# Kernel tuning notes

Hardware: AMD Instinct MI355X
Metric: run time of the kernel (lower is better)

The kernel has to match this reference:

```python
import jax, jax.numpy as jnp
import numpy as np

N_NODES = 50000
N_EDGES = 1_600_000
IN_DIM = 128
HID = 32
HEADS = 4
NEG_SLOPE = 0.2


def setup_inputs() -> dict:
    key = jax.random.key(0)
    ks = jax.random.split(key, 6)
    h = jax.random.normal(ks[0], (N_NODES, IN_DIM), dtype=jnp.float32)
    src = jax.random.randint(ks[1], (N_EDGES,), 0, N_NODES, dtype=jnp.int32)
    dst = jax.random.randint(ks[2], (N_EDGES,), 0, N_NODES, dtype=jnp.int32)
    s = 1.0 / np.sqrt(IN_DIM)  # ~ Linear default init scale
    Wq = (jax.random.normal(ks[3], (HEADS, IN_DIM, HID), dtype=jnp.float32) * s)
    Wk = (jax.random.normal(ks[4], (HEADS, IN_DIM, HID), dtype=jnp.float32) * s)
    Wv = (jax.random.normal(ks[5], (HEADS, IN_DIM, HID), dtype=jnp.float32) * s)
    return {"h": h, "src": src, "dst": dst, "Wq": Wq, "Wk": Wk, "Wv": Wv}


def _gat_forward(h, src, dst, Wq, Wk, Wv):
    n = h.shape[0]
    # per-head projections: [H, N, D]
    q = jnp.einsum('ni,hio->hno', h, Wq)
    k = jnp.einsum('ni,hio->hno', h, Wk)
    v = jnp.einsum('ni,hio->hno', h, Wv)
    # edge scores: e = leaky_relu(<q_src, k_dst>)  -> [H, E]
    e = jax.nn.leaky_relu(jnp.einsum('hed,hed->he', q[:, src], k[:, dst]),
                          negative_slope=NEG_SLOPE)
    # segment softmax over incoming edges of each dst node
    seg_max = jax.vmap(lambda x: jax.ops.segment_max(x, dst, num_segments=n))(e)
    seg_max = jax.lax.stop_gradient(jnp.where(jnp.isfinite(seg_max), seg_max, 0.0))
    ex = jnp.exp(e - seg_max[:, dst])                       # [H, E]
    denom = jax.vmap(lambda x: jax.ops.segment_sum(x, dst, num_segments=n))(ex)
    alpha = ex / jnp.maximum(denom, 1e-9)[:, dst]           # [H, E]
    # weighted scatter-sum of source values into dst nodes: [H, N, D]
    msg = alpha[..., None] * v[:, src]
    out = jax.vmap(lambda m: jax.ops.segment_sum(m, dst, num_segments=n))(msg)
    # concat heads along feature dim -> [N, H*D]
    return out.transpose(1, 0, 2).reshape(n, HEADS * HID)


def reference(h, src, dst, Wq, Wk, Wv):
    return _gat_forward(h, src, dst, Wq, Wk, Wv)
```

## Files before the change

### kernel.cpp

```cpp
#include <hip/hip_runtime.h>
#include <hip/hip_fp16.h>

#define IN_DIM 128
#define HID 32
#define HEADS 4
#define OUTC (HEADS*HID)
#define NEG_SLOPE 0.2f
#define BSH 4
#define BN 16
#define BCAP 768
#define NBMAX 3200
#define NCOLS 384
#define WPB 192
#define NP 25
#define PSH 11
#define PCAP 72704
#define PBLK 18
#define OSTRIDE 392

typedef _Float16 f16x8 __attribute__((ext_vector_type(8)));
typedef float    f32x4 __attribute__((ext_vector_type(4)));

__device__ __forceinline__ unsigned short f2h(float f) {
    return __half_as_ushort(__float2half_rn(f));
}
__device__ __forceinline__ float2 h2f2(unsigned u) {
    __half2 h = *reinterpret_cast<__half2*>(&u);
    return __half22float2(h);
}
__device__ __forceinline__ float qdot2(const uint2& w, const float4& kd) {
    float2 a = h2f2(w.x);
    float2 b = h2f2(w.y);
    return a.x * kd.x + a.y * kd.y + b.x * kd.z + b.y * kd.w;
}
__device__ __forceinline__ void vacc2(const uint2& w, float e, float4& acc) {
    float2 a = h2f2(w.x);
    float2 b = h2f2(w.y);
    acc.x = fmaf(e, a.x, acc.x);
    acc.y = fmaf(e, a.y, acc.y);
    acc.z = fmaf(e, b.x, acc.z);
    acc.w = fmaf(e, b.y, acc.w);
}

__device__ __forceinline__ void proj_body(
    char* smem_raw, int tid, int row0,
    const float* __restrict__ h, const unsigned short* __restrict__ Wt,
    unsigned short* __restrict__ K, unsigned short* __restrict__ Qa,
    unsigned short* __restrict__ Va, int n)
{
    unsigned short* hsm = (unsigned short*)smem_raw;

    for (int idx = tid; idx < 32 * 32; idx += 256) {
        int r  = idx >> 5;
        int c4 = idx & 31;
        int gr = row0 + r;
        float4 hv = (gr < n) ? ((const float4*)h)[(size_t)gr * 32 + c4]
                             : make_float4(0.f, 0.f, 0.f, 0.f);
        int sc = (c4 * 4) ^ ((r & 7) << 3);
        __half2 p01 = __floats2half2_rn(hv.x, hv.y);
        __half2 p23 = __floats2half2_rn(hv.z, hv.w);
        uint2 u;
        u.x = *(unsigned*)&p01;
        u.y = *(unsigned*)&p23;
        *(uint2*)&hsm[r * IN_DIM + sc] = u;
    }
    __syncthreads();

    const int w = tid >> 6;
    const int l = tid & 63;
    const int l15 = l & 15;
    const int kg  = l >> 4;
    const _Float16* Wt16 = (const _Float16*)Wt;

    f32x4 acc[2][6];
#pragma unroll
    for (int rt = 0; rt < 2; ++rt)
#pragma unroll
        for (int ct = 0; ct < 6; ++ct) acc[rt][ct] = (f32x4){0.f, 0.f, 0.f, 0.f};

#pragma unroll
    for (int s = 0; s < 4; ++s) {
        int scol = (s * 32 + kg * 8) ^ ((l & 7) << 3);
        f16x8 a0 = *(const f16x8*)&hsm[l15 * IN_DIM + scol];
        f16x8 a1 = *(const f16x8*)&hsm[(l15 + 16) * IN_DIM + scol];
#pragma unroll
        for (int ct = 0; ct < 6; ++ct) {
            int c = w * 96 + ct * 16 + l15;
            f16x8 b = *(const f16x8*)&Wt16[(size_t)c * IN_DIM + s * 32 + kg * 8];
            acc[0][ct] = __builtin_amdgcn_mfma_f32_16x16x32_f16(a0, b, acc[0][ct], 0, 0, 0);
            acc[1][ct] = __builtin_amdgcn_mfma_f32_16x16x32_f16(a1, b, acc[1][ct], 0, 0, 0);
        }
    }
    __syncthreads();

    unsigned short* osm = (unsigned short*)smem_raw;
#pragma unroll
    for (int rt = 0; rt < 2; ++rt) {
#pragma unroll
        for (int ct = 0; ct < 6; ++ct) {
            int cD = w * 96 + ct * 16 + l15;
#pragma unroll
            for (int r = 0; r < 4; ++r) {
                int rowl = rt * 16 + kg * 4 + r;
                osm[rowl * OSTRIDE + cD] = f2h(acc[rt][ct][r]);
            }
        }
    }
    __syncthreads();

    for (int c = tid; c < 32 * 96; c += 256) {
        int row  = c / 96;
        int col4 = c - row * 96;
        int node = row0 + row;
        if (node >= n) continue;
        uint2 v = *(const uint2*)&osm[row * OSTRIDE + col4 * 4];
        int colbase = col4 * 4;
        if (colbase < 128)
            *(uint2*)&K [(size_t)node * OUTC + colbase] = v;
        else if (colbase < 256)
            *(uint2*)&Qa[(size_t)node * OUTC + (colbase - 128)] = v;
        else
            *(uint2*)&Va[(size_t)node * OUTC + (colbase - 256)] = v;
    }
}

__global__ __launch_bounds__(256) void w_prep(
    const float* __restrict__ Wq, const float* __restrict__ Wk,
    const float* __restrict__ Wv, unsigned short* __restrict__ Wt,
    int* __restrict__ gcount, int* __restrict__ pcount)
{
    int idx = blockIdx.x * 256 + threadIdx.x;
    if (idx < NBMAX) gcount[idx] = 0;
    if (idx >= NBMAX && idx < NBMAX + NP) pcount[idx - NBMAX] = 0;
    if (idx >= NCOLS * IN_DIM) return;
    int c = idx >> 7, k = idx & 127;
    int sel = c >> 7;
    int cc  = c & 127;
    int head = cc >> 5, dcol = cc & 31;
    const float* W = (sel == 0) ? Wk : (sel == 1) ? Wq : Wv;
    Wt[idx] = f2h(W[(size_t)head * IN_DIM * HID + (size_t)k * HID + dcol]);
}

__global__ __launch_bounds__(256) void part_projA(
    const int* __restrict__ src, const int* __restrict__ dst,
    int* __restrict__ pcount, unsigned* __restrict__ ppairs,
    const float* __restrict__ h, const unsigned short* __restrict__ Wt,
    unsigned short* __restrict__ K, unsigned short* __restrict__ Qa,
    unsigned short* __restrict__ Va,
    int ne, int binblk, int n)
{
    __shared__ __align__(16) char smem_raw[32 * OSTRIDE * 2];
    const int tid = threadIdx.x;

    if ((int)blockIdx.x < binblk) {
        int* hist = (int*)smem_raw;
        int* base = hist + 32;
        const int bblk = blockIdx.x;

        if (tid < 32) hist[tid] = 0;
        __syncthreads();

        const int ne4 = ne >> 2;
        const int4* s4 = (const int4*)src;
        const int4* d4 = (const int4*)dst;

        int4 sv[4], dv[4];
        int loc[16], pk[16];
        bool val[4];
#pragma unroll
        for (int k2 = 0; k2 < 4; ++k2) {
            int idx = bblk * 1024 + k2 * 256 + tid;
            val[k2] = idx < ne4;
            if (val[k2]) { sv[k2] = s4[idx]; dv[k2] = d4[idx]; }
            else { sv[k2] = make_int4(0,0,0,0); dv[k2] = make_int4(0,0,0,0); }
        }
#pragma unroll
        for (int k2 = 0; k2 < 4; ++k2) {
            int dd[4] = { dv[k2].x, dv[k2].y, dv[k2].z, dv[k2].w };
#pragma unroll
            for (int j = 0; j < 4; ++j) {
                int p = dd[j] >> PSH;
                pk[k2*4+j]  = p;
                loc[k2*4+j] = val[k2] ? atomicAdd(&hist[p], 1) : 0;
            }
        }
        __syncthreads();
        if (tid < 32) base[tid] = hist[tid] ? atomicAdd(&pcount[tid], hist[tid]) : 0;
        __syncthreads();
#pragma unroll
        for (int k2 = 0; k2 < 4; ++k2) {
            if (!val[k2]) continue;
            int ss[4] = { sv[k2].x, sv[k2].y, sv[k2].z, sv[k2].w };
            int dd[4] = { dv[k2].x, dv[k2].y, dv[k2].z, dv[k2].w };
#pragma unroll
            for (int j = 0; j < 4; ++j) {
                int p   = pk[k2*4+j];
                int pos = base[p] + loc[k2*4+j];
                if (pos < PCAP)
                    ppairs[(size_t)p * PCAP + pos] =
                        ((unsigned)ss[j] << 16) | (unsigned)dd[j];
            }
        }
        if (bblk == 0 && tid == 0) {
            for (int e = ne4 * 4; e < ne; ++e) {
                int p   = dst[e] >> PSH;
                int pos = atomicAdd(&pcount[p], 1);
                if (pos < PCAP)
                    ppairs[(size_t)p * PCAP + pos] =
                        ((unsigned)src[e] << 16) | (unsigned)dst[e];
            }
        }
        return;
    }

    proj_body(smem_raw, tid, (blockIdx.x - binblk) * 32, h, Wt, K, Qa, Va, n);
}

__global__ __launch_bounds__(256) void pass2_projB(
    const unsigned* __restrict__ ppairs, const int* __restrict__ pcount,
    int* __restrict__ gcount, unsigned* __restrict__ pairs,
    const float* __restrict__ h, const unsigned short* __restrict__ Wt,
    unsigned short* __restrict__ K, unsigned short* __restrict__ Qa,
    unsigned short* __restrict__ Va,
    int p2blk, int rowbase, int n)
{
    __shared__ __align__(16) char smem_raw[32 * OSTRIDE * 2];
    const int tid = threadIdx.x;

    if ((int)blockIdx.x < p2blk) {
        int* hist = (int*)smem_raw;
        int* base = hist + 128;
        const int p = blockIdx.x / PBLK;
        const int c = blockIdx.x % PBLK;

        int mp = pcount[p]; if (mp > PCAP) mp = PCAP;
        const int i0 = c * 4096;
        if (i0 >= mp) return;
        const int iend = min(i0 + 4096, mp);

        if (tid < 128) hist[tid] = 0;
        __syncthreads();

        const unsigned* pp = ppairs + (size_t)p * PCAP;
        unsigned rec[16];
        int loc[16], lb[16];
#pragma unroll
        for (int k = 0; k < 16; ++k) {
            int i = i0 + k * 256 + tid;
            if (i < iend) {
                unsigned r = pp[i];
                rec[k] = r;
                int b = ((r & 0xFFFFu) >> BSH) & 127;
                lb[k]  = b;
                loc[k] = atomicAdd(&hist[b], 1);
            } else {
                rec[k] = 0; lb[k] = -1; loc[k] = 0;
            }
        }
        __syncthreads();
        if (tid < 128)
            base[tid] = hist[tid] ? atomicAdd(&gcount[p * 128 + tid], hist[tid]) : 0;
        __syncthreads();
#pragma unroll
        for (int k = 0; k < 16; ++k) {
            if (lb[k] < 0) continue;
            unsigned r = rec[k];
            int gb  = p * 128 + lb[k];
            int pos = base[lb[k]] + loc[k];
            if (pos < BCAP)
                pairs[(size_t)gb * BCAP + pos] =
                    ((r >> 16) << BSH) | (r & (BN - 1));
        }
        return;
    }

    proj_body(smem_raw, tid, (blockIdx.x - p2blk) * 32 + rowbase,
              h, Wt, K, Qa, Va, n);
}

__global__ __launch_bounds__(256) void gat_bucket(
    const unsigned* __restrict__ pairs, const int* __restrict__ gcount,
    const uint2* __restrict__ Q2, const uint2* __restrict__ V2,
    const ushort4* __restrict__ K4,
    float* __restrict__ out, int n, int nbuck)
{
    __shared__ unsigned short sl[BCAP];
    __shared__ float exls[BCAP * 4];
    __shared__ int cl[BN], cur[BN], off[BN + 1];

    const int b = blockIdx.x;
    if (b >= nbuck) return;
    const int tid = threadIdx.x;

    if (tid < BN) cl[tid] = 0;
    __syncthreads();

    int m = gcount[b]; if (m > BCAP) m = BCAP;
    const unsigned* pb = pairs + (size_t)b * BCAP;

    for (int i = tid; i < m; i += 256) atomicAdd(&cl[pb[i] & (BN - 1)], 1);
    __syncthreads();
    if (tid == 0) {
        int a = 0;
#pragma unroll
        for (int i = 0; i < BN; ++i) { off[i] = a; cur[i] = a; a += cl[i]; }
        off[BN] = a;
    }
    __syncthreads();
    for (int i = tid; i < m; i += 256) {
        unsigned p = pb[i];
        int pos = atomicAdd(&cur[p & (BN - 1)], 1);
        sl[pos] = (unsigned short)(p >> BSH);
    }
    __syncthreads();

    const int gi   = tid >> 5;
    const int l32  = tid & 31;
    const int hsel = l32 >> 3;
    const bool wr  = (l32 & 7) == 0;

    float dsum[BN / 8];

#pragma unroll
    for (int q = 0; q < BN / 8; ++q) {
        int nl   = q * 8 + gi;
        int node = b * BN + nl;
        float ds = 0.f;
        if (node < n) {
            ushort4 kh = K4[(size_t)node * 32 + l32];
            float2 k01 = h2f2(*(unsigned*)&kh.x);
            float2 k23 = h2f2(*(unsigned*)&kh.z);
            const float4 kd = make_float4(k01.x, k01.y, k23.x, k23.y);

            int j        = off[nl];
            const int je = off[nl + 1];
            for (; j + 3 < je; j += 4) {
                int s0 = sl[j], s1 = sl[j + 1], s2 = sl[j + 2], s3 = sl[j + 3];
                uint2 w0 = Q2[(size_t)s0 * 32 + l32];
                uint2 w1 = Q2[(size_t)s1 * 32 + l32];
                uint2 w2 = Q2[(size_t)s2 * 32 + l32];
                uint2 w3 = Q2[(size_t)s3 * 32 + l32];
                float p0 = qdot2(w0, kd), p1 = qdot2(w1, kd);
                float p2 = qdot2(w2, kd), p3 = qdot2(w3, kd);
#pragma unroll
                for (int o = 1; o < 8; o <<= 1) {
                    p0 += __shfl_xor(p0, o, 8);
                    p1 += __shfl_xor(p1, o, 8);
                    p2 += __shfl_xor(p2, o, 8);
                    p3 += __shfl_xor(p3, o, 8);
                }
                float e0 = __expf(p0 > 0.f ? p0 : NEG_SLOPE * p0);
                float e1 = __expf(p1 > 0.f ? p1 : NEG_SLOPE * p1);
                float e2 = __expf(p2 > 0.f ? p2 : NEG_SLOPE * p2);
                float e3 = __expf(p3 > 0.f ? p3 : NEG_SLOPE * p3);
                ds += (e0 + e1) + (e2 + e3);
                if (wr) {
                    exls[(j    ) * 4 + hsel] = e0;
                    exls[(j + 1) * 4 + hsel] = e1;
                    exls[(j + 2) * 4 + hsel] = e2;
                    exls[(j + 3) * 4 + hsel] = e3;
                }
            }
            for (; j < je; ++j) {
                int s0 = sl[j];
                uint2 w0 = Q2[(size_t)s0 * 32 + l32];
                float p0 = qdot2(w0, kd);
#pragma unroll
                for (int o = 1; o < 8; o <<= 1) p0 += __shfl_xor(p0, o, 8);
                float e0 = __expf(p0 > 0.f ? p0 : NEG_SLOPE * p0);
                ds += e0;
                if (wr) exls[j * 4 + hsel] = e0;
            }
        }
        dsum[q] = ds;
    }
    __syncthreads();

#pragma unroll
    for (int q = 0; q < BN / 8; ++q) {
        int nl   = q * 8 + gi;
        int node = b * BN + nl;
        if (node >= n) continue;

        int j        = off[nl];
        const int je = off[nl + 1];
        float4 acc = make_float4(0.f, 0.f, 0.f, 0.f);

        for (; j + 3 < je; j += 4) {
            int s0 = sl[j], s1 = sl[j + 1], s2 = sl[j + 2], s3 = sl[j + 3];
            uint2 w0 = V2[(size_t)s0 * 32 + l32];
            uint2 w1 = V2[(size_t)s1 * 32 + l32];
            uint2 w2 = V2[(size_t)s2 * 32 + l32];
            uint2 w3 = V2[(size_t)s3 * 32 + l32];
            float e0 = exls[(j    ) * 4 + hsel];
            float e1 = exls[(j + 1) * 4 + hsel];
            float e2 = exls[(j + 2) * 4 + hsel];
            float e3 = exls[(j + 3) * 4 + hsel];
            vacc2(w0, e0, acc); vacc2(w1, e1, acc);
            vacc2(w2, e2, acc); vacc2(w3, e3, acc);
        }
        for (; j < je; ++j) {
            int s0 = sl[j];
            uint2 w0 = V2[(size_t)s0 * 32 + l32];
            float e0 = exls[j * 4 + hsel];
            vacc2(w0, e0, acc);
        }

        float inv = 1.f / fmaxf(dsum[q], 1e-9f);
        float4 o; o.x = acc.x*inv; o.y = acc.y*inv; o.z = acc.z*inv; o.w = acc.w*inv;
        ((float4*)out)[(size_t)node * 32 + l32] = o;
    }
}

extern "C" void kernel_launch(void* const* d_in, const int* in_sizes, int n_in,
                              void* d_out, int out_size, void* d_ws, size_t ws_size,
                              hipStream_t stream) {
    const float* h   = (const float*)d_in[0];
    const int*   src = (const int*)d_in[1];
    const int*   dst = (const int*)d_in[2];
    const float* Wq  = (const float*)d_in[3];
    const float* Wk  = (const float*)d_in[4];
    const float* Wv  = (const float*)d_in[5];
    float* out = (float*)d_out;

    const int n     = in_sizes[0] / IN_DIM;
    const int ne    = in_sizes[1];
    const int nbuck = (n + BN - 1) >> BSH;

    unsigned short* K      = (unsigned short*)d_ws;
    unsigned short* Qa     = K  + (size_t)n * OUTC;
    unsigned short* Va     = Qa + (size_t)n * OUTC;
    int*            gcount = (int*)(Va + (size_t)n * OUTC);
    int*            pcount = gcount + NBMAX;
    unsigned*       ppairs = (unsigned*)(pcount + 64);
    unsigned*       pairs  = ppairs + (size_t)NP * PCAP;
    unsigned short* Wt     = (unsigned short*)(pairs + (size_t)NBMAX * BCAP);

    w_prep<<<WPB, 256, 0, stream>>>(Wq, Wk, Wv, Wt, gcount, pcount);

    int ne4     = ne >> 2;
    int binblk  = (ne4 + 1023) / 1024;
    int projblk = (n + 31) / 32;
    int projA   = (projblk + 1) / 2;
    int projB   = projblk - projA;

    part_projA<<<binblk + projA, 256, 0, stream>>>(
        src, dst, pcount, ppairs, h, Wt, K, Qa, Va, ne, binblk, n);

    int p2blk = NP * PBLK;
    pass2_projB<<<p2blk + projB, 256, 0, stream>>>(
        ppairs, pcount, gcount, pairs, h, Wt, K, Qa, Va,
        p2blk, projA * 32, n);

    gat_bucket<<<nbuck, 256, 0, stream>>>(pairs, gcount, (const uint2*)Qa,
                                          (const uint2*)Va, (const ushort4*)K,
                                          out, n, nbuck);
}
```

Measured before the change: 165.0 us.

## Sort bucket edges by source-range sub-bucket to synchronize Q/V gather locality

Each dst bucket's edges are now also sorted into 8 sub-segments keyed by the high bits of the source node index. All warps in the block sweep the sub-segments in lockstep, with a block barrier after each one. The aim is to keep Q and V gathers from concurrent warps within a narrower source-node range, which should improve L2/cache locality. The cost is 16 extra __syncthreads per block, a serial scan over 128 counters done by one thread, and possible load imbalance between warps inside each sub-step.

```diff
diff --git a/kernel.cpp b/kernel.cpp
--- a/kernel.cpp
+++ b/kernel.cpp
@@ -17,6 +17,7 @@
 #define PCAP 72704
 #define PBLK 18
 #define OSTRIDE 392
+#define NSB 8
 
 typedef _Float16 f16x8 __attribute__((ext_vector_type(8)));
 typedef float    f32x4 __attribute__((ext_vector_type(4)));
@@ -286,31 +287,35 @@
 {
     __shared__ unsigned short sl[BCAP];
     __shared__ float exls[BCAP * 4];
-    __shared__ int cl[BN], cur[BN], off[BN + 1];
+    __shared__ int cl[BN * NSB], cur[BN * NSB], off[BN * NSB + 1];
 
     const int b = blockIdx.x;
     if (b >= nbuck) return;
     const int tid = threadIdx.x;
 
-    if (tid < BN) cl[tid] = 0;
+    for (int i = tid; i < BN * NSB; i += 256) cl[i] = 0;
     __syncthreads();
 
     int m = gcount[b]; if (m > BCAP) m = BCAP;
     const unsigned* pb = pairs + (size_t)b * BCAP;
 
-    for (int i = tid; i < m; i += 256) atomicAdd(&cl[pb[i] & (BN - 1)], 1);
+    for (int i = tid; i < m; i += 256) {
+        unsigned r = pb[i];
+        int seg = (int)(r & (BN - 1)) * NSB + (int)(r >> (BSH + 13));
+        atomicAdd(&cl[seg], 1);
+    }
     __syncthreads();
     if (tid == 0) {
         int a = 0;
-#pragma unroll
-        for (int i = 0; i < BN; ++i) { off[i] = a; cur[i] = a; a += cl[i]; }
-        off[BN] = a;
+        for (int i = 0; i < BN * NSB; ++i) { off[i] = a; cur[i] = a; a += cl[i]; }
+        off[BN * NSB] = a;
     }
     __syncthreads();
     for (int i = tid; i < m; i += 256) {
-        unsigned p = pb[i];
-        int pos = atomicAdd(&cur[p & (BN - 1)], 1);
-        sl[pos] = (unsigned short)(p >> BSH);
+        unsigned r = pb[i];
+        int seg = (int)(r & (BN - 1)) * NSB + (int)(r >> (BSH + 13));
+        int pos = atomicAdd(&cur[seg], 1);
+        sl[pos] = (unsigned short)(r >> BSH);
     }
     __syncthreads();
 
@@ -319,21 +324,31 @@
     const int hsel = l32 >> 3;
     const bool wr  = (l32 & 7) == 0;
 
-    float dsum[BN / 8];
-
-#pragma unroll
-    for (int q = 0; q < BN / 8; ++q) {
-        int nl   = q * 8 + gi;
-        int node = b * BN + nl;
-        float ds = 0.f;
+    float4 kdv[2];
+    float  dsum[2] = {0.f, 0.f};
+#pragma unroll
+    for (int q = 0; q < 2; ++q) {
+        int node = b * BN + q * 8 + gi;
         if (node < n) {
             ushort4 kh = K4[(size_t)node * 32 + l32];
             float2 k01 = h2f2(*(unsigned*)&kh.x);
             float2 k23 = h2f2(*(unsigned*)&kh.z);
-            const float4 kd = make_float4(k01.x, k01.y, k23.x, k23.y);
-
-            int j        = off[nl];
-            const int je = off[nl + 1];
+            kdv[q] = make_float4(k01.x, k01.y, k23.x, k23.y);
+        } else {
+            kdv[q] = make_float4(0.f, 0.f, 0.f, 0.f);
+        }
+    }
+
+    for (int sb = 0; sb < NSB; ++sb) {
+#pragma unroll
+        for (int q = 0; q < 2; ++q) {
+            int nl   = q * 8 + gi;
+            int node = b * BN + nl;
+            if (node >= n) continue;
+            const float4 kd = kdv[q];
+            int j        = off[nl * NSB + sb];
+            const int je = off[nl * NSB + sb + 1];
+            float ds = 0.f;
             for (; j + 3 < je; j += 4) {
                 int s0 = sl[j], s1 = sl[j + 1], s2 = sl[j + 2], s3 = sl[j + 3];
                 uint2 w0 = Q2[(size_t)s0 * 32 + l32];
@@ -371,43 +386,54 @@
                 ds += e0;
                 if (wr) exls[j * 4 + hsel] = e0;
             }
-        }
-        dsum[q] = ds;
-    }
-    __syncthreads();
-
-#pragma unroll
-    for (int q = 0; q < BN / 8; ++q) {
-        int nl   = q * 8 + gi;
-        int node = b * BN + nl;
+            dsum[q] += ds;
+        }
+        __syncthreads();
+    }
+
+    float4 acc[2];
+    acc[0] = make_float4(0.f, 0.f, 0.f, 0.f);
+    acc[1] = make_float4(0.f, 0.f, 0.f, 0.f);
+
+    for (int sb = 0; sb < NSB; ++sb) {
+#pragma unroll
+        for (int q = 0; q < 2; ++q) {
+            int nl   = q * 8 + gi;
+            int node = b * BN + nl;
+            if (node >= n) continue;
+            int j        = off[nl * NSB + sb];
+            const int je = off[nl * NSB + sb + 1];
+            for (; j + 3 < je; j += 4) {
+                int s0 = sl[j], s1 = sl[j + 1], s2 = sl[j + 2], s3 = sl[j + 3];
+                uint2 w0 = V2[(size_t)s0 * 32 + l32];
+                uint2 w1 = V2[(size_t)s1 * 32 + l32];
+                uint2 w2 = V2[(size_t)s2 * 32 + l32];
+                uint2 w3 = V2[(size_t)s3 * 32 + l32];
+                float e0 = exls[(j    ) * 4 + hsel];
+                float e1 = exls[(j + 1) * 4 + hsel];
+                float e2 = exls[(j + 2) * 4 + hsel];
+                float e3 = exls[(j + 3) * 4 + hsel];
+                vacc2(w0, e0, acc[q]); vacc2(w1, e1, acc[q]);
+                vacc2(w2, e2, acc[q]); vacc2(w3, e3, acc[q]);
+            }
+            for (; j < je; ++j) {
+                int s0 = sl[j];
+                uint2 w0 = V2[(size_t)s0 * 32 + l32];
+                float e0 = exls[j * 4 + hsel];
+                vacc2(w0, e0, acc[q]);
+            }
+        }
+        __syncthreads();
+    }
+
+#pragma unroll
+    for (int q = 0; q < 2; ++q) {
+        int node = b * BN + q * 8 + gi;
         if (node >= n) continue;
-
-        int j        = off[nl];
-        const int je = off[nl + 1];
-        float4 acc = make_float4(0.f, 0.f, 0.f, 0.f);
-
-        for (; j + 3 < je; j += 4) {
-            int s0 = sl[j], s1 = sl[j + 1], s2 = sl[j + 2], s3 = sl[j + 3];
-            uint2 w0 = V2[(size_t)s0 * 32 + l32];
-            uint2 w1 = V2[(size_t)s1 * 32 + l32];
-            uint2 w2 = V2[(size_t)s2 * 32 + l32];
-            uint2 w3 = V2[(size_t)s3 * 32 + l32];
-            float e0 = exls[(j    ) * 4 + hsel];
-            float e1 = exls[(j + 1) * 4 + hsel];
-            float e2 = exls[(j + 2) * 4 + hsel];
-            float e3 = exls[(j + 3) * 4 + hsel];
-            vacc2(w0, e0, acc); vacc2(w1, e1, acc);
-            vacc2(w2, e2, acc); vacc2(w3, e3, acc);
-        }
-        for (; j < je; ++j) {
-            int s0 = sl[j];
-            uint2 w0 = V2[(size_t)s0 * 32 + l32];
-            float e0 = exls[j * 4 + hsel];
-            vacc2(w0, e0, acc);
-        }
-
         float inv = 1.f / fmaxf(dsum[q], 1e-9f);
-        float4 o; o.x = acc.x*inv; o.y = acc.y*inv; o.z = acc.z*inv; o.w = acc.w*inv;
+        float4 o;
+        o.x = acc[q].x * inv; o.y = acc[q].y * inv;
+        o.z = acc[q].z * inv; o.w = acc[q].w * inv;
         ((float4*)out)[(size_t)node * 32 + l32] = o;
     }
 }
```

After: 195.8 us. +18.7%, slower.
